# Performance work log

Hardware: AMD Instinct MI355X
Metric: run time of the kernel (lower is better)

## Reference

```python
import jax, jax.numpy as jnp
import numpy as np

KERNEL_MUL = 2.0
KERNEL_NUM = 5


def setup_inputs() -> dict:
    key = jax.random.key(0)
    k1, k2 = jax.random.split(key)
    N, D = 8192, 256
    subggroup = jax.random.randint(k1, (N, 1), 0, 2, dtype=jnp.int64)
    outputs = jax.random.normal(k2, (N, D), dtype=jnp.float32)
    return {"subggroup": subggroup, "outputs": outputs}


def reference(subggroup, outputs):
    # Binary labels: rows with label 0 form `source` (Min), label 1 form `target` (Maj).
    # concat(source, target) is a permutation of `outputs`, so we compute the
    # full NxN multi-RBF kernel once and take masked means -- identical math.
    sub = subggroup[:, 0]
    m0 = (sub == 0).astype(outputs.dtype)  # source mask
    m1 = (sub == 1).astype(outputs.dtype)  # target mask
    n = outputs.shape[0]

    # Pairwise squared L2 distances via matmul (fused cdist), [N, N]
    sq = jnp.sum(outputs * outputs, axis=-1)
    L2 = jnp.maximum(sq[:, None] + sq[None, :] - 2.0 * (outputs @ outputs.T), 0.0)

    # bandwidth computed from detached distances (torch uses L2_distance.data)
    bandwidth = jax.lax.stop_gradient(jnp.sum(L2)) / (n * n - n)
    bandwidth = bandwidth / (KERNEL_MUL ** (KERNEL_NUM // 2))

    K = jnp.zeros_like(L2)
    for i in range(KERNEL_NUM):
        K = K + jnp.exp(-L2 / (bandwidth * (KERNEL_MUL ** i)))

    n0 = jnp.sum(m0)
    n1 = jnp.sum(m1)
    XX = jnp.einsum('i,ij,j->', m0, K, m0) / (n0 * n0)
    YY = jnp.einsum('i,ij,j->', m1, K, m1) / (n1 * n1)
    XY = jnp.einsum('i,ij,j->', m0, K, m1) / (n0 * n1)
    YX = jnp.einsum('i,ij,j->', m1, K, m0) / (n1 * n0)
    return XX + YY - XY - YX
```

## Files before the change

kernel.cpp:

```cpp
#include <hip/hip_runtime.h>

#define N_ROWS 8192
#define DIMS   256
#define NRT    128
#define NCT    64
#define NFULL  2048
#define NCHUNK 2112
#define K1B    256
#define K3B    1024

typedef _Float16 f16x4 __attribute__((ext_vector_type(4)));
typedef _Float16 f16x8 __attribute__((ext_vector_type(8)));
typedef float   f32x16 __attribute__((ext_vector_type(16)));

#define WS_PLANE  0
#define WS_SQ     (4 * 1024 * 1024)
#define WS_RED    (WS_SQ + 32768)
#define WS_SSQA   (WS_RED + 1024)
#define WS_N0A    (WS_SSQA + 4)
#define WS_SC     (WS_N0A + 4)
#define WS_PART   (WS_RED + 2048)

struct Scalars {
    unsigned int ctr;
    unsigned int t3;
};

#define BL(dst, p, o) asm volatile("global_load_dwordx4 %0, %1, off offset:" o \
                                   : "=v"(dst) : "v"(p))

__global__ __launch_bounds__(256) void k1_rows(const float* __restrict__ x,
                                               const long long* __restrict__ sub,
                                               float* __restrict__ sq,
                                               float* __restrict__ colsumA,
                                               float* __restrict__ ssqA,
                                               unsigned int* __restrict__ n0A,
                                               unsigned short* __restrict__ plane) {
    __shared__ _Float16 stg[16 * 512];
    __shared__ float cls[4][256];
    __shared__ float smq[4];
    const int t = threadIdx.x;
    const int l = t & 63;
    const int w = t >> 6;
    const int base = blockIdx.x * 32;

    float4 colacc = make_float4(0.f, 0.f, 0.f, 0.f);
    float  my_sumsq = 0.f;

    const int ks  = l >> 2;
    const int shi = ((l >> 1) & 1) * 32;
    const int j4  = (l & 1) * 4;

    #pragma unroll
    for (int r = 0; r < 8; ++r) {
        const int rr  = w * 8 + r;
        const int row = base + rr;
        const float4 v = ((const float4*)(x + (size_t)row * DIMS))[l];
        colacc.x += v.x; colacc.y += v.y; colacc.z += v.z; colacc.w += v.w;

        f16x4 h = { (_Float16)v.x, (_Float16)v.y, (_Float16)v.z, (_Float16)v.w };
        *(f16x4*)&stg[ks * 512 + (rr + shi) * 8 + j4] = h;

        float s = v.x * v.x + v.y * v.y + v.z * v.z + v.w * v.w;
        #pragma unroll
        for (int off = 32; off; off >>= 1) s += __shfl_down(s, off, 64);
        if (l == 0) { sq[row] = s; my_sumsq += s; }
    }
    if (l == 0) smq[w] = my_sumsq;
    *(float4*)&cls[w][l * 4] = colacc;
    __syncthreads();

    {
        const uint4* src = (const uint4*)stg;
        uint4* dst = (uint4*)(plane + (size_t)blockIdx.x * 8192);
        #pragma unroll
        for (int i = 0; i < 4; ++i) dst[i * 256 + t] = src[i * 256 + t];
    }

    atomicAdd(&colsumA[t], cls[0][t] + cls[1][t] + cls[2][t] + cls[3][t]);
    if (t == 0) atomicAdd(ssqA, smq[0] + smq[1] + smq[2] + smq[3]);
    if (w == 1) {
        unsigned long long m1 = __ballot(l < 32 && (int)sub[base + l] == 0);
        if (l == 0) atomicAdd(n0A, (unsigned int)__popcll(m1));
    }
}

__global__ __launch_bounds__(256, 2) void k3_mmd(const unsigned short* __restrict__ plane,
                                                 const long long* __restrict__ sub,
                                                 const float* __restrict__ sq,
                                                 const float* __restrict__ colsumA,
                                                 const float* __restrict__ ssqA,
                                                 const unsigned int* __restrict__ n0A,
                                                 Scalars* sc,
                                                 double* __restrict__ partial,
                                                 float* __restrict__ out) {
    __shared__ char ldsA[32768];
    __shared__ float2 sqwI[64];
    __shared__ double dd[4];
    __shared__ unsigned int qb;

    const int t  = threadIdx.x;
    const int l  = t & 63;
    const int w  = t >> 6;
    const int lh = l >> 5;
    const int ln = l & 31;

    float c2, w0, w1;
    {
        const float4 c4 = ((const float4*)colsumA)[l];
        float cs2 = c4.x * c4.x + c4.y * c4.y + c4.z * c4.z + c4.w * c4.w;
        #pragma unroll
        for (int off = 32; off; off >>= 1) cs2 += __shfl_xor(cs2, off, 64);
        const float ssq = *ssqA;
        const float n0f = (float)*n0A;
        const double n = (double)N_ROWS;
        const double sumL2 = 2.0 * n * (double)ssq - 2.0 * (double)cs2;
        const double bw = sumL2 / (n * n - n) / 4.0;
        c2 = (float)(-1.4426950408889634 / (16.0 * bw));
        const double n0 = (double)n0f, n1 = n - n0;
        w0 = (float)( 1.0 / n0);
        w1 = (float)(-1.0 / n1);
    }

    double dsum = 0.0;
    f16x8 b[16];

    if (t == 0) qb = atomicAdd(&sc->ctr, 1u);
    for (;;) {
        __syncthreads();
        const unsigned q0 = qb;
        if (q0 >= NCHUNK) break;
        int ri, cj, nt;
        if (q0 < NFULL) {
            int q = (int)q0; ri = 0;
            for (;;) { const int fc = (NCT - (ri >> 1)) >> 1; if (q < fc) break; q -= fc; ++ri; }
            cj = (ri >> 1) + 2 * q;
            nt = 2;
        } else {
            const int s = (int)(q0 - NFULL);
            const int bb = 2 * (s >> 1) + 1;
            ri = 2 * bb + (s & 1);
            cj = NCT - 1;
            nt = 1;
        }

        #pragma unroll
        for (int i = 0; i < 8; ++i) {
            const unsigned short* g = plane + (((size_t)(ri * 32 + w * 8 + i)) << 9) + (l << 3);
            char* lp = ldsA + ((w * 8 + i) << 10);
            __builtin_amdgcn_global_load_lds(
                (const __attribute__((address_space(1))) unsigned int*)(const void*)g,
                (__attribute__((address_space(3))) unsigned int*)(void*)lp, 16, 0, 0);
        }
        if (t < 64) {
            const int I = ri * 64 + t;
            sqwI[t] = make_float2(sq[I], ((int)sub[I] == 0) ? w0 : w1);
        }
        {
            const unsigned short* p0 = plane + (((size_t)(cj * 4 + w) * 16) << 9) + (l << 3);
            const unsigned short* p1 = p0 + 2048;
            const unsigned short* p2 = p0 + 4096;
            const unsigned short* p3 = p0 + 6144;
            BL(b[0], p0,"0"); BL(b[1], p0,"1024"); BL(b[2], p0,"2048"); BL(b[3], p0,"3072");
            BL(b[4], p1,"0"); BL(b[5], p1,"1024"); BL(b[6], p1,"2048"); BL(b[7], p1,"3072");
            BL(b[8], p2,"0"); BL(b[9], p2,"1024"); BL(b[10],p2,"2048"); BL(b[11],p2,"3072");
            BL(b[12],p3,"0"); BL(b[13],p3,"1024"); BL(b[14],p3,"2048"); BL(b[15],p3,"3072");
        }
        const int J0 = cj * 128 + w * 32 + ln;
        float sJ  = sq[J0];
        float wJv = ((int)sub[J0] == 0) ? w0 : w1;
        __syncthreads();

        for (int tt = 0; tt < nt; ++tt) {
            const int cjt = cj + tt;
            const bool dg = (cjt == (ri >> 1));
            asm volatile("s_waitcnt vmcnt(0)" ::: "memory");
            __builtin_amdgcn_sched_barrier(0);

            f32x16 acc[2] = {};
            #pragma unroll
            for (int ks = 0; ks < 16; ++ks) {
                #pragma unroll
                for (int m = 0; m < 2; ++m) {
                    const f16x8 a = *(const f16x8*)(ldsA + ((m * 16 + ks) << 10) + (l << 4));
                    acc[m] = __builtin_amdgcn_mfma_f32_32x32x16_f16(a, b[ks], acc[m], 0, 0, 0);
                }
            }

            if (tt == nt - 1 && t == 0) qb = atomicAdd(&sc->ctr, 1u);

            float sJn = 0.f, wJn = 0.f;
            if (tt + 1 < nt) {
                const unsigned short* p0 = plane + (((size_t)((cjt + 1) * 4 + w) * 16) << 9) + (l << 3);
                const unsigned short* p1 = p0 + 2048;
                const unsigned short* p2 = p0 + 4096;
                const unsigned short* p3 = p0 + 6144;
                BL(b[0], p0,"0"); BL(b[1], p0,"1024"); BL(b[2], p0,"2048"); BL(b[3], p0,"3072");
                BL(b[4], p1,"0"); BL(b[5], p1,"1024"); BL(b[6], p1,"2048"); BL(b[7], p1,"3072");
                BL(b[8], p2,"0"); BL(b[9], p2,"1024"); BL(b[10],p2,"2048"); BL(b[11],p2,"3072");
                BL(b[12],p3,"0"); BL(b[13],p3,"1024"); BL(b[14],p3,"2048"); BL(b[15],p3,"3072");
                const int Jn = (cjt + 1) * 128 + w * 32 + ln;
                sJn = sq[Jn];
                wJn = ((int)sub[Jn] == 0) ? w0 : w1;
            }

            float part = 0.f;
            #pragma unroll
            for (int m = 0; m < 2; ++m) {
                #pragma unroll
                for (int r = 0; r < 16; ++r) {
                    const int Il = m * 32 + (r & 3) + ((r >> 2) << 3) + (lh << 2);
                    const float2 pi = sqwI[Il];
                    float l2 = fmaxf(pi.x + sJ - 2.f * acc[m][r], 0.f);
                    const float e  = __builtin_amdgcn_exp2f(l2 * c2);
                    const float e2 = e * e, e4 = e2 * e2, e8 = e4 * e4;
                    const float K  = ((e + e2) + (e4 + e8)) + e8 * e8;
                    float w2 = pi.y * wJv;
                    if (dg) {
                        const int Ig = ri * 64 + Il;
                        const int Jg = cjt * 128 + w * 32 + ln;
                        w2 *= (Ig < Jg) ? 2.f : ((Ig == Jg) ? 1.f : 0.f);
                    }
                    part = fmaf(K, w2, part);
                }
            }
            dsum += (double)part * (dg ? 1.0 : 2.0);
            sJ = sJn; wJv = wJn;
        }
    }

    #pragma unroll
    for (int off = 32; off; off >>= 1) dsum += __shfl_down(dsum, off, 64);
    __syncthreads();
    if (l == 0) dd[w] = dsum;
    __syncthreads();
    if (t == 0) {
        partial[blockIdx.x] = dd[0] + dd[1] + dd[2] + dd[3];
        __threadfence();
        qb = (atomicAdd(&sc->t3, 1u) == K3B - 1) ? 1u : 0u;
    }
    __syncthreads();
    if (qb) {
        __threadfence();
        double v = partial[t] + partial[t + 256] + partial[t + 512] + partial[t + 768];
        #pragma unroll
        for (int off = 32; off; off >>= 1) v += __shfl_down(v, off, 64);
        if (l == 0) dd[w] = v;
        __syncthreads();
        if (t == 0) out[0] = (float)(dd[0] + dd[1] + dd[2] + dd[3]);
    }
}

extern "C" void kernel_launch(void* const* d_in, const int* in_sizes, int n_in,
                              void* d_out, int out_size, void* d_ws, size_t ws_size,
                              hipStream_t stream) {
    const long long* sub = (const long long*)d_in[0];
    const float*     x   = (const float*)d_in[1];
    float* out = (float*)d_out;

    char* ws = (char*)d_ws;
    unsigned short* plane   = (unsigned short*)(ws + WS_PLANE);
    float*          sq      = (float*)(ws + WS_SQ);
    float*          colsumA = (float*)(ws + WS_RED);
    float*          ssqA    = (float*)(ws + WS_SSQA);
    unsigned int*   n0A     = (unsigned int*)(ws + WS_N0A);
    Scalars*        sc      = (Scalars*)(ws + WS_SC);
    double*         partial = (double*)(ws + WS_PART);

    hipMemsetAsync(ws + WS_RED, 0, 1040, stream);
    k1_rows<<<K1B, 256, 0, stream>>>(x, sub, sq, colsumA, ssqA, n0A, plane);
    k3_mmd<<<K3B, 256, 0, stream>>>(plane, sub, sq, colsumA, ssqA, n0A, sc, partial, out);
}
```

Baseline: 138.7 us.

## Split B-fragment register buffer in half to raise occupancy to four blocks

The per-wave B operand buffer shrinks from 16 to 8 f16x8 registers. The K loop is split into two halves, and the second half of B is reloaded from global memory between them. Launch bounds go from 2 to 4 blocks per SM so more waves can hide latency. In exchange, each tile now has a serialized global-load wait in the middle of its MFMA loop, and LDS use per CU grows with the extra resident blocks.

```diff
diff --git a/kernel.cpp b/kernel.cpp
--- a/kernel.cpp
+++ b/kernel.cpp
@@ -2,7 +2,6 @@
 
 #define N_ROWS 8192
 #define DIMS   256
-#define NRT    128
 #define NCT    64
 #define NFULL  2048
 #define NCHUNK 2112
@@ -85,7 +84,7 @@
     }
 }
 
-__global__ __launch_bounds__(256, 2) void k3_mmd(const unsigned short* __restrict__ plane,
+__global__ __launch_bounds__(256, 4) void k3_mmd(const unsigned short* __restrict__ plane,
                                                  const long long* __restrict__ sub,
                                                  const float* __restrict__ sq,
                                                  const float* __restrict__ colsumA,
@@ -123,7 +122,15 @@
     }
 
     double dsum = 0.0;
-    f16x8 b[16];
+    f16x8 b[8];
+    float sJ = 0.f, wJv = 0.f;
+
+    auto issueB = [&](int cj_, int h) {
+        const unsigned short* p0 = plane + (((size_t)(cj_ * 4 + w) * 16 + h * 8) << 9) + (l << 3);
+        const unsigned short* p1 = p0 + 2048;
+        BL(b[0], p0,"0"); BL(b[1], p0,"1024"); BL(b[2], p0,"2048"); BL(b[3], p0,"3072");
+        BL(b[4], p1,"0"); BL(b[5], p1,"1024"); BL(b[6], p1,"2048"); BL(b[7], p1,"3072");
+    };
 
     if (t == 0) qb = atomicAdd(&sc->ctr, 1u);
     for (;;) {
@@ -145,9 +152,10 @@
         }
 
         #pragma unroll
-        for (int i = 0; i < 8; ++i) {
-            const unsigned short* g = plane + (((size_t)(ri * 32 + w * 8 + i)) << 9) + (l << 3);
-            char* lp = ldsA + ((w * 8 + i) << 10);
+        for (int j = 0; j < 8; ++j) {
+            const int i = w * 8 + j;
+            const unsigned short* g = plane + (((size_t)ri * 32 + i) << 9) + (l << 3);
+            char* lp = ldsA + (i << 10);
             __builtin_amdgcn_global_load_lds(
                 (const __attribute__((address_space(1))) unsigned int*)(const void*)g,
                 (__attribute__((address_space(3))) unsigned int*)(void*)lp, 16, 0, 0);
@@ -156,19 +164,10 @@
             const int I = ri * 64 + t;
             sqwI[t] = make_float2(sq[I], ((int)sub[I] == 0) ? w0 : w1);
         }
-        {
-            const unsigned short* p0 = plane + (((size_t)(cj * 4 + w) * 16) << 9) + (l << 3);
-            const unsigned short* p1 = p0 + 2048;
-            const unsigned short* p2 = p0 + 4096;
-            const unsigned short* p3 = p0 + 6144;
-            BL(b[0], p0,"0"); BL(b[1], p0,"1024"); BL(b[2], p0,"2048"); BL(b[3], p0,"3072");
-            BL(b[4], p1,"0"); BL(b[5], p1,"1024"); BL(b[6], p1,"2048"); BL(b[7], p1,"3072");
-            BL(b[8], p2,"0"); BL(b[9], p2,"1024"); BL(b[10],p2,"2048"); BL(b[11],p2,"3072");
-            BL(b[12],p3,"0"); BL(b[13],p3,"1024"); BL(b[14],p3,"2048"); BL(b[15],p3,"3072");
-        }
+        issueB(cj, 0);
         const int J0 = cj * 128 + w * 32 + ln;
-        float sJ  = sq[J0];
-        float wJv = ((int)sub[J0] == 0) ? w0 : w1;
+        sJ  = sq[J0];
+        wJv = ((int)sub[J0] == 0) ? w0 : w1;
         __syncthreads();
 
         for (int tt = 0; tt < nt; ++tt) {
@@ -179,26 +178,30 @@
 
             f32x16 acc[2] = {};
             #pragma unroll
-            for (int ks = 0; ks < 16; ++ks) {
-                #pragma unroll
-                for (int m = 0; m < 2; ++m) {
-                    const f16x8 a = *(const f16x8*)(ldsA + ((m * 16 + ks) << 10) + (l << 4));
-                    acc[m] = __builtin_amdgcn_mfma_f32_32x32x16_f16(a, b[ks], acc[m], 0, 0, 0);
-                }
-            }
+            for (int ks = 0; ks < 8; ++ks) {
+                const f16x8 a0 = *(const f16x8*)(ldsA + ((0 * 16 + ks) << 10) + (l << 4));
+                const f16x8 a1 = *(const f16x8*)(ldsA + ((1 * 16 + ks) << 10) + (l << 4));
+                acc[0] = __builtin_amdgcn_mfma_f32_32x32x16_f16(a0, b[ks], acc[0], 0, 0, 0);
+                acc[1] = __builtin_amdgcn_mfma_f32_32x32x16_f16(a1, b[ks], acc[1], 0, 0, 0);
+            }
+            __builtin_amdgcn_sched_barrier(0);
+            issueB(cjt, 1);
+            asm volatile("s_waitcnt vmcnt(0)" ::: "memory");
+            __builtin_amdgcn_sched_barrier(0);
+            #pragma unroll
+            for (int ks = 0; ks < 8; ++ks) {
+                const f16x8 a0 = *(const f16x8*)(ldsA + ((0 * 16 + 8 + ks) << 10) + (l << 4));
+                const f16x8 a1 = *(const f16x8*)(ldsA + ((1 * 16 + 8 + ks) << 10) + (l << 4));
+                acc[0] = __builtin_amdgcn_mfma_f32_32x32x16_f16(a0, b[ks], acc[0], 0, 0, 0);
+                acc[1] = __builtin_amdgcn_mfma_f32_32x32x16_f16(a1, b[ks], acc[1], 0, 0, 0);
+            }
+            __builtin_amdgcn_sched_barrier(0);
 
             if (tt == nt - 1 && t == 0) qb = atomicAdd(&sc->ctr, 1u);
 
             float sJn = 0.f, wJn = 0.f;
             if (tt + 1 < nt) {
-                const unsigned short* p0 = plane + (((size_t)((cjt + 1) * 4 + w) * 16) << 9) + (l << 3);
-                const unsigned short* p1 = p0 + 2048;
-                const unsigned short* p2 = p0 + 4096;
-                const unsigned short* p3 = p0 + 6144;
-                BL(b[0], p0,"0"); BL(b[1], p0,"1024"); BL(b[2], p0,"2048"); BL(b[3], p0,"3072");
-                BL(b[4], p1,"0"); BL(b[5], p1,"1024"); BL(b[6], p1,"2048"); BL(b[7], p1,"3072");
-                BL(b[8], p2,"0"); BL(b[9], p2,"1024"); BL(b[10],p2,"2048"); BL(b[11],p2,"3072");
-                BL(b[12],p3,"0"); BL(b[13],p3,"1024"); BL(b[14],p3,"2048"); BL(b[15],p3,"3072");
+                issueB(cjt + 1, 0);
                 const int Jn = (cjt + 1) * 128 + w * 32 + ln;
                 sJn = sq[Jn];
                 wJn = ((int)sub[Jn] == 0) ? w0 : w1;
```

Result: slower. 181.5 us (+30.9%).
